# Performance work log

Measured on AMD Instinct MI355X. Metric: run time of the kernel, lower is better.

## Reference

```python
import jax, jax.numpy as jnp
import numpy as np

HIDDEN = 1024
NUM_HEADS = 16
HEAD_DIM = 64
B, S = 2, 2048


def setup_inputs() -> dict:
    key = jax.random.key(0)
    k1, k2, k3 = jax.random.split(key, 3)
    x = jax.random.normal(k1, (B, S, HIDDEN), dtype=jnp.float32)
    # xavier-uniform style scaling for the projection weights
    lim_qkv = (6.0 / (HIDDEN + 3 * NUM_HEADS * HEAD_DIM)) ** 0.5
    lim_o = (6.0 / (NUM_HEADS * HEAD_DIM + HIDDEN)) ** 0.5
    w_qkv = jax.random.uniform(k2, (HIDDEN, 3 * NUM_HEADS * HEAD_DIM), jnp.float32, -lim_qkv, lim_qkv)
    w_o = jax.random.uniform(k3, (NUM_HEADS * HEAD_DIM, HIDDEN), jnp.float32, -lim_o, lim_o)
    return {"x": x, "w_qkv": w_qkv, "w_o": w_o}


def reference(x, w_qkv, w_o):
    b, s, _ = x.shape
    qkv = jnp.einsum('bsh,hf->bsf', x, w_qkv)               # [b, s, 3*H*D]
    qkv = qkv.reshape(b, s, 3, NUM_HEADS, HEAD_DIM)
    q = jnp.transpose(qkv[:, :, 0], (0, 2, 1, 3))           # [b, h, s, d]
    k = jnp.transpose(qkv[:, :, 1], (0, 2, 3, 1))           # [b, h, d, s]
    v = jnp.transpose(qkv[:, :, 2], (0, 2, 1, 3))           # [b, h, s, d]
    scores = jnp.einsum('bhqd,bhdk->bhqk', q, k) / jnp.sqrt(jnp.float32(HEAD_DIM))
    scores = jax.nn.softmax(scores, axis=-1)                # [b, h, q, k]
    # NOTE: faithful to source bug: sums over q, output indexed by k
    values = jnp.einsum('bhqk,bhkd->bhkd', scores, v)       # [b, h, s, d]
    values = jnp.transpose(values, (0, 2, 1, 3)).reshape(b, s, NUM_HEADS * HEAD_DIM)
    return jnp.einsum('bsf,fh->bsh', values, w_o)
```

## Files before the change

kernel.cpp:

```cpp
#include <hip/hip_runtime.h>
#include <stdint.h>


#define DEV static __device__ __forceinline__

typedef unsigned short u16;
typedef __attribute__((ext_vector_type(4))) float f32x4;
typedef __attribute__((ext_vector_type(16))) float f32x16;
typedef __bf16 bf16x8 __attribute__((ext_vector_type(8)));
typedef __attribute__((ext_vector_type(8))) unsigned short u16x8;
typedef __attribute__((ext_vector_type(4))) unsigned short u16x4;

#define QSCALE 0.18033688011112042f

DEV u16 f2bf(float f) {
    unsigned u = __builtin_bit_cast(unsigned, f);
    u += 0x7fffu + ((u >> 16) & 1u);
    return (u16)(u >> 16);
}
DEV float bf2f(u16 h) {
    unsigned u = ((unsigned)h) << 16;
    return __builtin_bit_cast(float, u);
}

DEV void async_copy16(const void* g, void* l) {
    __builtin_amdgcn_global_load_lds(
        (__attribute__((address_space(1))) void*)(g),
        (__attribute__((address_space(3))) void*)(l), 16, 0, 0);
}


__global__ __launch_bounds__(256) void cast_f32_bf16(
    const float* __restrict__ src, u16* __restrict__ dst, int n4) {
    int i = blockIdx.x * 256 + threadIdx.x;
    if (i >= n4) return;
    f32x4 v = *(const f32x4*)(src + (size_t)i * 4);
    u16x4 o;
#pragma unroll
    for (int j = 0; j < 4; j++) o[j] = f2bf(v[j]);
    *(u16x4*)(dst + (size_t)i * 4) = o;
}

__global__ __launch_bounds__(256) void transpose_cast(
    const float* __restrict__ src, u16* __restrict__ dst, int rows, int cols) {
    __shared__ float tile[32][33];
    int c0 = blockIdx.x * 32, r0 = blockIdx.y * 32;
    int tx = threadIdx.x, ty = threadIdx.y;
#pragma unroll
    for (int i = 0; i < 4; i++)
        tile[ty + i * 8][tx] = src[(size_t)(r0 + ty + i * 8) * cols + c0 + tx];
    __syncthreads();
#pragma unroll
    for (int i = 0; i < 4; i++)
        dst[(size_t)(c0 + ty + i * 8) * rows + r0 + tx] = f2bf(tile[tx][ty + i * 8]);
}

DEV void gemm128_core(const u16* __restrict__ A, const u16* __restrict__ Bt,
                      int m0, int n0, int Kdim, u16* As, u16* Bs,
                      f32x4 (*acc)[4]) {
    const int t = threadIdx.x;
    const int wave = t >> 6;
    const int lane = t & 63;
    const int quad = lane >> 4;
    const int l16 = lane & 15;
    const int wr = wave >> 1;
    const int wc = wave & 1;

    for (int kt = 0; kt < Kdim; kt += 32) {
#pragma unroll
        for (int i = 0; i < 2; i++) {
            int idx = i * 256 + t;
            int row = idx >> 2, kc = idx & 3;
            async_copy16(A + (size_t)(m0 + row) * Kdim + kt + kc * 8, &As[idx * 8]);
            async_copy16(Bt + (size_t)(n0 + row) * Kdim + kt + kc * 8, &Bs[idx * 8]);
        }
        __syncthreads();
        bf16x8 af[4], bfr[4];
#pragma unroll
        for (int mt = 0; mt < 4; mt++)
            af[mt] = *(const bf16x8*)&As[(wr * 64 + mt * 16 + l16) * 32 + quad * 8];
#pragma unroll
        for (int nt = 0; nt < 4; nt++)
            bfr[nt] = *(const bf16x8*)&Bs[(wc * 64 + nt * 16 + l16) * 32 + quad * 8];
#pragma unroll
        for (int mt = 0; mt < 4; mt++)
#pragma unroll
            for (int nt = 0; nt < 4; nt++)
                acc[mt][nt] = __builtin_amdgcn_mfma_f32_16x16x32_bf16(
                    af[mt], bfr[nt], acc[mt][nt], 0, 0, 0);
        __syncthreads();
    }
}

__global__ __launch_bounds__(256) void gemm_qkv(
    const u16* __restrict__ A, const u16* __restrict__ Bt,
    u16* __restrict__ qb, u16* __restrict__ kb, u16* __restrict__ vb) {
    __shared__ __align__(16) u16 As[128 * 32];
    __shared__ __align__(16) u16 Bs[128 * 32];
    const int m0 = blockIdx.y * 128;
    const int n0 = blockIdx.x * 128;
    f32x4 acc[4][4];
#pragma unroll
    for (int i = 0; i < 4; i++)
#pragma unroll
        for (int j = 0; j < 4; j++) acc[i][j] = {0.f, 0.f, 0.f, 0.f};

    gemm128_core(A, Bt, m0, n0, 1024, As, Bs, acc);

    const int t = threadIdx.x;
    const int wave = t >> 6, lane = t & 63;
    const int quad = lane >> 4, l16 = lane & 15;
    const int wr = wave >> 1, wc = wave & 1;
#pragma unroll
    for (int nt = 0; nt < 4; nt++) {
        int nn = n0 + wc * 64 + nt * 16 + l16;
        int tsel = nn >> 10;
        int rem = nn & 1023;
        int h = rem >> 6, d = rem & 63;
        u16* dst = tsel == 0 ? qb : (tsel == 1 ? kb : vb);
        float scl = tsel == 0 ? QSCALE : 1.0f;
#pragma unroll
        for (int mt = 0; mt < 4; mt++) {
#pragma unroll
            for (int r = 0; r < 4; r++) {
                int mm = m0 + wr * 64 + mt * 16 + quad * 4 + r;
                int b = mm >> 11, s = mm & 2047;
                dst[(size_t)((b * 16 + h) * 2048 + s) * 64 + d] = f2bf(acc[mt][nt][r] * scl);
            }
        }
    }
}

__global__ __launch_bounds__(256) void gemm_out(
    const u16* __restrict__ A, const u16* __restrict__ Bt,
    float* __restrict__ out) {
    __shared__ __align__(16) u16 As[128 * 32];
    __shared__ __align__(16) u16 Bs[128 * 32];
    const int m0 = blockIdx.y * 128;
    const int n0 = blockIdx.x * 128;
    f32x4 acc[4][4];
#pragma unroll
    for (int i = 0; i < 4; i++)
#pragma unroll
        for (int j = 0; j < 4; j++) acc[i][j] = {0.f, 0.f, 0.f, 0.f};

    gemm128_core(A, Bt, m0, n0, 1024, As, Bs, acc);

    const int t = threadIdx.x;
    const int wave = t >> 6, lane = t & 63;
    const int quad = lane >> 4, l16 = lane & 15;
    const int wr = wave >> 1, wc = wave & 1;
#pragma unroll
    for (int nt = 0; nt < 4; nt++) {
        int nn = n0 + wc * 64 + nt * 16 + l16;
#pragma unroll
        for (int mt = 0; mt < 4; mt++) {
#pragma unroll
            for (int r = 0; r < 4; r++) {
                int mm = m0 + wr * 64 + mt * 16 + quad * 4 + r;
                out[(size_t)mm * 1024 + nn] = acc[mt][nt][r];
            }
        }
    }
}

__global__ __launch_bounds__(256) void attn_pass1(
    const u16* __restrict__ qb, const u16* __restrict__ kb,
    float* __restrict__ lp) {
    __shared__ __align__(16) u16 Ks0[64 * 32];
    __shared__ __align__(16) u16 Ks1[64 * 32];
    const int t = threadIdx.x;
    const int wave = t >> 6;
    const int lane = t & 63;
    const int l32 = lane & 31, half = lane >> 5;
    const int kchunk = blockIdx.x & 1;
    const int qblk = (blockIdx.x >> 1) & 15;
    const int bh = blockIdx.x >> 5;
    const int q0 = qblk * 128 + wave * 32;

    const u16* Qr = qb + (size_t)(bh * 2048 + q0 + l32) * 64 + half * 8;
    bf16x8 a[4];
#pragma unroll
    for (int f = 0; f < 4; f++) a[f] = *(const bf16x8*)&Qr[f * 16];

    const u16* Kbase = kb + (size_t)(bh * 2048 + kchunk * 1024) * 64;
    const int srow = t >> 2, sc = (t & 3) * 8;

    float lsum[16];
#pragma unroll
    for (int r = 0; r < 16; r++) lsum[r] = 0.f;

    for (int kt = 0; kt < 16; kt++) {
        const u16* src = Kbase + (size_t)(kt * 64 + srow) * 64 + sc;
        async_copy16(src, &Ks0[t * 8]);
        async_copy16(src + 32, &Ks1[t * 8]);
        __syncthreads();
#pragma unroll
        for (int sub = 0; sub < 2; sub++) {
            const int row = sub * 32 + l32;
            bf16x8 bfr[4];
            bfr[0] = *(const bf16x8*)&Ks0[row * 32 + half * 8];
            bfr[1] = *(const bf16x8*)&Ks0[row * 32 + 16 + half * 8];
            bfr[2] = *(const bf16x8*)&Ks1[row * 32 + half * 8];
            bfr[3] = *(const bf16x8*)&Ks1[row * 32 + 16 + half * 8];
            f32x16 acc;
#pragma unroll
            for (int r = 0; r < 16; r++) acc[r] = 0.f;
#pragma unroll
            for (int f = 0; f < 4; f++)
                acc = __builtin_amdgcn_mfma_f32_32x32x16_bf16(a[f], bfr[f], acc, 0, 0, 0);
#pragma unroll
            for (int r = 0; r < 16; r++)
                lsum[r] += __builtin_amdgcn_exp2f(acc[r]);
        }
        __syncthreads();
    }
#pragma unroll
    for (int r = 0; r < 16; r++) {
        float v = lsum[r];
        v += __shfl_xor(v, 1);
        v += __shfl_xor(v, 2);
        v += __shfl_xor(v, 4);
        v += __shfl_xor(v, 8);
        v += __shfl_xor(v, 16);
        lsum[r] = v;
    }
    if (l32 == 0) {
        float* dst = lp + kchunk * 65536 + bh * 2048 + q0 + half * 4;
#pragma unroll
        for (int r = 0; r < 16; r++)
            dst[(r & 3) + 8 * (r >> 2)] = lsum[r];
    }
}

__global__ __launch_bounds__(256) void reduce_li(
    const float* __restrict__ lp, float* __restrict__ li) {
    int i = blockIdx.x * 256 + threadIdx.x;
    li[i] = 1.0f / (lp[i] + lp[65536 + i]);
}

__global__ __launch_bounds__(256) void attn_pass2(
    const u16* __restrict__ qb, const u16* __restrict__ kb,
    const float* __restrict__ li_ws, float* __restrict__ cp) {
    __shared__ __align__(16) u16 Qs0[64 * 32];
    __shared__ __align__(16) u16 Qs1[64 * 32];
    const int t = threadIdx.x;
    const int wave = t >> 6;
    const int lane = t & 63;
    const int l32 = lane & 31, half = lane >> 5;
    const int qchunk = blockIdx.x & 1;
    const int kblk = (blockIdx.x >> 1) & 15;
    const int bh = blockIdx.x >> 5;
    const int k0 = kblk * 128 + wave * 32;

    const u16* Kr = kb + (size_t)(bh * 2048 + k0 + l32) * 64 + half * 8;
    bf16x8 b[4];
#pragma unroll
    for (int f = 0; f < 4; f++) b[f] = *(const bf16x8*)&Kr[f * 16];

    const u16* Qbase = qb + (size_t)(bh * 2048 + qchunk * 1024) * 64;
    const float* li_b = li_ws + bh * 2048 + qchunk * 1024;
    const int srow = t >> 2, sc = (t & 3) * 8;

    float cs = 0.f;

    for (int qt = 0; qt < 16; qt++) {
        const u16* src = Qbase + (size_t)(qt * 64 + srow) * 64 + sc;
        async_copy16(src, &Qs0[t * 8]);
        async_copy16(src + 32, &Qs1[t * 8]);
        __syncthreads();
#pragma unroll
        for (int sub = 0; sub < 2; sub++) {
            const int row = sub * 32 + l32;
            bf16x8 af[4];
            af[0] = *(const bf16x8*)&Qs0[row * 32 + half * 8];
            af[1] = *(const bf16x8*)&Qs0[row * 32 + 16 + half * 8];
            af[2] = *(const bf16x8*)&Qs1[row * 32 + half * 8];
            af[3] = *(const bf16x8*)&Qs1[row * 32 + 16 + half * 8];
            f32x16 acc;
#pragma unroll
            for (int r = 0; r < 16; r++) acc[r] = 0.f;
#pragma unroll
            for (int f = 0; f < 4; f++)
                acc = __builtin_amdgcn_mfma_f32_32x32x16_bf16(af[f], b[f], acc, 0, 0, 0);
            const float* lr = li_b + qt * 64 + sub * 32 + half * 4;
            f32x4 li0 = *(const f32x4*)&lr[0];
            f32x4 li1 = *(const f32x4*)&lr[8];
            f32x4 li2 = *(const f32x4*)&lr[16];
            f32x4 li3 = *(const f32x4*)&lr[24];
#pragma unroll
            for (int r = 0; r < 4; r++) cs += __builtin_amdgcn_exp2f(acc[r]) * li0[r];
#pragma unroll
            for (int r = 0; r < 4; r++) cs += __builtin_amdgcn_exp2f(acc[4 + r]) * li1[r];
#pragma unroll
            for (int r = 0; r < 4; r++) cs += __builtin_amdgcn_exp2f(acc[8 + r]) * li2[r];
#pragma unroll
            for (int r = 0; r < 4; r++) cs += __builtin_amdgcn_exp2f(acc[12 + r]) * li3[r];
        }
        __syncthreads();
    }
    cs += __shfl_xor(cs, 32);
    if (lane < 32)
        cp[qchunk * 65536 + bh * 2048 + k0 + lane] = cs;
}

__global__ __launch_bounds__(256) void scale_v(
    const u16* __restrict__ vb, const float* __restrict__ cp,
    u16* __restrict__ valsb) {
    int tid = blockIdx.x * 256 + threadIdx.x;
    int base = tid << 3;
    int bh = base >> 17;
    int rem = base & 131071;
    int s = rem >> 6;
    int d0 = rem & 63;
    int ci = bh * 2048 + s;
    float cs = cp[ci] + cp[65536 + ci];
    u16x8 v = *(const u16x8*)(vb + (size_t)base);
    u16x8 o;
#pragma unroll
    for (int i = 0; i < 8; i++) o[i] = f2bf(bf2f(v[i]) * cs);
    int b = bh >> 4, h = bh & 15;
    *(u16x8*)(valsb + (size_t)((b * 2048 + s) * 1024) + h * 64 + d0) = o;
}


extern "C" void kernel_launch(void* const* d_in, const int* in_sizes, int n_in,
                              void* d_out, int out_size, void* d_ws, size_t ws_size,
                              hipStream_t stream) {
    const float* x    = (const float*)d_in[0];
    const float* wqkv = (const float*)d_in[1];
    const float* wo   = (const float*)d_in[2];
    float* out = (float*)d_out;
    char* ws = (char*)d_ws;

    u16* xb      = (u16*)(ws);
    u16* wqkvT   = (u16*)(ws + 8388608);
    u16* woT     = (u16*)(ws + 14680064);
    u16* qb      = (u16*)(ws + 16777216);
    u16* kb      = (u16*)(ws + 25165824);
    u16* vb      = (u16*)(ws + 33554432);
    float* li_ws = (float*)(ws + 41943040);
    u16* valsb   = (u16*)(ws + 42467328);
    float* lp    = (float*)(ws);
    float* cp    = (float*)(ws + 1048576);

    cast_f32_bf16<<<4096, 256, 0, stream>>>(x, xb, 1048576);
    transpose_cast<<<dim3(96, 32), dim3(32, 8), 0, stream>>>(wqkv, wqkvT, 1024, 3072);
    transpose_cast<<<dim3(32, 32), dim3(32, 8), 0, stream>>>(wo, woT, 1024, 1024);
    gemm_qkv<<<dim3(24, 32), 256, 0, stream>>>(xb, wqkvT, qb, kb, vb);
    attn_pass1<<<1024, 256, 0, stream>>>(qb, kb, lp);
    reduce_li<<<256, 256, 0, stream>>>(lp, li_ws);
    attn_pass2<<<1024, 256, 0, stream>>>(qb, kb, li_ws, cp);
    scale_v<<<2048, 256, 0, stream>>>(vb, cp, valsb);
    gemm_out<<<dim3(8, 32), 256, 0, stream>>>(valsb, woT, out);
}
```

Measured before the change: 209.3 us.

## Fuse reciprocal row-sum into pass2, enlarge attention tiles, shrink output GEMM tiles

The separate reduce_li kernel is removed. Each attn_pass2 block now computes 1/(lp0+lp1) for its 1024 queries into LDS and reads it from there instead of from global memory. Both attention passes stage 128 rows of K/Q per iteration instead of 64, which halves the number of loop iterations and barriers. gemm_out switches to 64x128 tiles with its own inline loop, doubling the grid to 512 blocks for better CU occupancy, at the cost of less data reuse per block.

```diff
diff --git a/kernel.cpp b/kernel.cpp
--- a/kernel.cpp
+++ b/kernel.cpp
@@ -134,30 +134,53 @@
 __global__ __launch_bounds__(256) void gemm_out(
     const u16* __restrict__ A, const u16* __restrict__ Bt,
     float* __restrict__ out) {
-    __shared__ __align__(16) u16 As[128 * 32];
+    __shared__ __align__(16) u16 As[64 * 32];
     __shared__ __align__(16) u16 Bs[128 * 32];
-    const int m0 = blockIdx.y * 128;
+    const int m0 = blockIdx.y * 64;
     const int n0 = blockIdx.x * 128;
-    f32x4 acc[4][4];
-#pragma unroll
-    for (int i = 0; i < 4; i++)
-#pragma unroll
-        for (int j = 0; j < 4; j++) acc[i][j] = {0.f, 0.f, 0.f, 0.f};
-
-    gemm128_core(A, Bt, m0, n0, 1024, As, Bs, acc);
-
     const int t = threadIdx.x;
     const int wave = t >> 6, lane = t & 63;
     const int quad = lane >> 4, l16 = lane & 15;
     const int wr = wave >> 1, wc = wave & 1;
+
+    f32x4 acc[2][4];
+#pragma unroll
+    for (int i = 0; i < 2; i++)
+#pragma unroll
+        for (int j = 0; j < 4; j++) acc[i][j] = {0.f, 0.f, 0.f, 0.f};
+
+    for (int kt = 0; kt < 1024; kt += 32) {
+        async_copy16(A + (size_t)(m0 + (t >> 2)) * 1024 + kt + (t & 3) * 8, &As[t * 8]);
+#pragma unroll
+        for (int i = 0; i < 2; i++) {
+            int idx = i * 256 + t;
+            int row = idx >> 2, kc = idx & 3;
+            async_copy16(Bt + (size_t)(n0 + row) * 1024 + kt + kc * 8, &Bs[idx * 8]);
+        }
+        __syncthreads();
+        bf16x8 af[2], bfr[4];
+#pragma unroll
+        for (int mt = 0; mt < 2; mt++)
+            af[mt] = *(const bf16x8*)&As[(wr * 32 + mt * 16 + l16) * 32 + quad * 8];
+#pragma unroll
+        for (int nt = 0; nt < 4; nt++)
+            bfr[nt] = *(const bf16x8*)&Bs[(wc * 64 + nt * 16 + l16) * 32 + quad * 8];
+#pragma unroll
+        for (int mt = 0; mt < 2; mt++)
+#pragma unroll
+            for (int nt = 0; nt < 4; nt++)
+                acc[mt][nt] = __builtin_amdgcn_mfma_f32_16x16x32_bf16(
+                    af[mt], bfr[nt], acc[mt][nt], 0, 0, 0);
+        __syncthreads();
+    }
 #pragma unroll
     for (int nt = 0; nt < 4; nt++) {
         int nn = n0 + wc * 64 + nt * 16 + l16;
 #pragma unroll
-        for (int mt = 0; mt < 4; mt++) {
+        for (int mt = 0; mt < 2; mt++) {
 #pragma unroll
             for (int r = 0; r < 4; r++) {
-                int mm = m0 + wr * 64 + mt * 16 + quad * 4 + r;
+                int mm = m0 + wr * 32 + mt * 16 + quad * 4 + r;
                 out[(size_t)mm * 1024 + nn] = acc[mt][nt][r];
             }
         }
@@ -167,8 +190,8 @@
 __global__ __launch_bounds__(256) void attn_pass1(
     const u16* __restrict__ qb, const u16* __restrict__ kb,
     float* __restrict__ lp) {
-    __shared__ __align__(16) u16 Ks0[64 * 32];
-    __shared__ __align__(16) u16 Ks1[64 * 32];
+    __shared__ __align__(16) u16 Ks0[128 * 32];
+    __shared__ __align__(16) u16 Ks1[128 * 32];
     const int t = threadIdx.x;
     const int wave = t >> 6;
     const int lane = t & 63;
@@ -190,13 +213,16 @@
 #pragma unroll
     for (int r = 0; r < 16; r++) lsum[r] = 0.f;
 
-    for (int kt = 0; kt < 16; kt++) {
-        const u16* src = Kbase + (size_t)(kt * 64 + srow) * 64 + sc;
-        async_copy16(src, &Ks0[t * 8]);
-        async_copy16(src + 32, &Ks1[t * 8]);
-        __syncthreads();
-#pragma unroll
-        for (int sub = 0; sub < 2; sub++) {
+    for (int kt = 0; kt < 8; kt++) {
+#pragma unroll
+        for (int rr = 0; rr < 2; rr++) {
+            const u16* src = Kbase + (size_t)(kt * 128 + rr * 64 + srow) * 64 + sc;
+            async_copy16(src, &Ks0[rr * 2048 + t * 8]);
+            async_copy16(src + 32, &Ks1[rr * 2048 + t * 8]);
+        }
+        __syncthreads();
+#pragma unroll
+        for (int sub = 0; sub < 4; sub++) {
             const int row = sub * 32 + l32;
             bf16x8 bfr[4];
             bfr[0] = *(const bf16x8*)&Ks0[row * 32 + half * 8];
@@ -233,17 +259,12 @@
     }
 }
 
-__global__ __launch_bounds__(256) void reduce_li(
-    const float* __restrict__ lp, float* __restrict__ li) {
-    int i = blockIdx.x * 256 + threadIdx.x;
-    li[i] = 1.0f / (lp[i] + lp[65536 + i]);
-}
-
 __global__ __launch_bounds__(256) void attn_pass2(
     const u16* __restrict__ qb, const u16* __restrict__ kb,
-    const float* __restrict__ li_ws, float* __restrict__ cp) {
-    __shared__ __align__(16) u16 Qs0[64 * 32];
-    __shared__ __align__(16) u16 Qs1[64 * 32];
+    const float* __restrict__ lp, float* __restrict__ cp) {
+    __shared__ __align__(16) u16 Qs0[128 * 32];
+    __shared__ __align__(16) u16 Qs1[128 * 32];
+    __shared__ __align__(16) float li_lds[1024];
     const int t = threadIdx.x;
     const int wave = t >> 6;
     const int lane = t & 63;
@@ -253,24 +274,37 @@
     const int bh = blockIdx.x >> 5;
     const int k0 = kblk * 128 + wave * 32;
 
+    {
+        const int base = bh * 2048 + qchunk * 1024;
+        f32x4 p0 = *(const f32x4*)&lp[base + t * 4];
+        f32x4 p1 = *(const f32x4*)&lp[65536 + base + t * 4];
+        f32x4 li;
+#pragma unroll
+        for (int j = 0; j < 4; j++) li[j] = 1.0f / (p0[j] + p1[j]);
+        *(f32x4*)&li_lds[t * 4] = li;
+    }
+
     const u16* Kr = kb + (size_t)(bh * 2048 + k0 + l32) * 64 + half * 8;
     bf16x8 b[4];
 #pragma unroll
     for (int f = 0; f < 4; f++) b[f] = *(const bf16x8*)&Kr[f * 16];
 
     const u16* Qbase = qb + (size_t)(bh * 2048 + qchunk * 1024) * 64;
-    const float* li_b = li_ws + bh * 2048 + qchunk * 1024;
     const int srow = t >> 2, sc = (t & 3) * 8;
 
     float cs = 0.f;
-
-    for (int qt = 0; qt < 16; qt++) {
-        const u16* src = Qbase + (size_t)(qt * 64 + srow) * 64 + sc;
-        async_copy16(src, &Qs0[t * 8]);
-        async_copy16(src + 32, &Qs1[t * 8]);
-        __syncthreads();
-#pragma unroll
-        for (int sub = 0; sub < 2; sub++) {
+    __syncthreads();
+
+    for (int qt = 0; qt < 8; qt++) {
+#pragma unroll
+        for (int rr = 0; rr < 2; rr++) {
+            const u16* src = Qbase + (size_t)(qt * 128 + rr * 64 + srow) * 64 + sc;
+            async_copy16(src, &Qs0[rr * 2048 + t * 8]);
+            async_copy16(src + 32, &Qs1[rr * 2048 + t * 8]);
+        }
+        __syncthreads();
+#pragma unroll
+        for (int sub = 0; sub < 4; sub++) {
             const int row = sub * 32 + l32;
             bf16x8 af[4];
             af[0] = *(const bf16x8*)&Qs0[row * 32 + half * 8];
@@ -283,7 +317,7 @@
 #pragma unroll
             for (int f = 0; f < 4; f++)
                 acc = __builtin_amdgcn_mfma_f32_32x32x16_bf16(af[f], b[f], acc, 0, 0, 0);
-            const float* lr = li_b + qt * 64 + sub * 32 + half * 4;
+            const float* lr = &li_lds[qt * 128 + sub * 32 + half * 4];
             f32x4 li0 = *(const f32x4*)&lr[0];
             f32x4 li1 = *(const f32x4*)&lr[8];
             f32x4 li2 = *(const f32x4*)&lr[16];
@@ -339,7 +373,6 @@
     u16* qb      = (u16*)(ws + 16777216);
     u16* kb      = (u16*)(ws + 25165824);
     u16* vb      = (u16*)(ws + 33554432);
-    float* li_ws = (float*)(ws + 41943040);
     u16* valsb   = (u16*)(ws + 42467328);
     float* lp    = (float*)(ws);
     float* cp    = (float*)(ws + 1048576);
@@ -349,8 +382,7 @@
     transpose_cast<<<dim3(32, 32), dim3(32, 8), 0, stream>>>(wo, woT, 1024, 1024);
     gemm_qkv<<<dim3(24, 32), 256, 0, stream>>>(xb, wqkvT, qb, kb, vb);
     attn_pass1<<<1024, 256, 0, stream>>>(qb, kb, lp);
-    reduce_li<<<256, 256, 0, stream>>>(lp, li_ws);
-    attn_pass2<<<1024, 256, 0, stream>>>(qb, kb, li_ws, cp);
+    attn_pass2<<<1024, 256, 0, stream>>>(qb, kb, lp, cp);
     scale_v<<<2048, 256, 0, stream>>>(vb, cp, valsb);
-    gemm_out<<<dim3(8, 32), 256, 0, stream>>>(valsb, woT, out);
-}
+    gemm_out<<<dim3(8, 64), 256, 0, stream>>>(valsb, woT, out);
+}
```

Measured after the change: 200.5 us. 4.2% less time.
